# Kernel optimization log

Measured on AMD Instinct MI355X. Metric: run time of the kernel, lower is better.

The kernel has to match this reference:

```python
import jax, jax.numpy as jnp
import numpy as np

B, S, D, H = 2, 2048, 1024, 16
HD = D // H  # head_dim = 64


def setup_inputs() -> dict:
    key = jax.random.key(0)
    ks = jax.random.split(key, 5)
    scale = 0.02
    return {
        "x": jax.random.normal(ks[0], (B, S, D), dtype=jnp.float32),
        "q_w": jax.random.normal(ks[1], (D, D), dtype=jnp.float32) * scale,
        "k_w": jax.random.normal(ks[2], (D, D), dtype=jnp.float32) * scale,
        "v_w": jax.random.normal(ks[3], (D, D), dtype=jnp.float32) * scale,
        "o_w": jax.random.normal(ks[4], (D, D), dtype=jnp.float32) * scale,
    }


def _mhsa(x, q_w, k_w, v_w, o_w):
    b, s, d = x.shape
    # projections: weight is [out, in] as in torch Parameter usage
    Q = jnp.einsum('bsd,kd->bsk', x, q_w)
    K = jnp.einsum('bsd,kd->bsk', x, k_w)
    V = jnp.einsum('bsd,kd->bsk', x, v_w)
    # split heads: b s (h hd) -> b h s hd
    Q = Q.reshape(b, s, H, HD).transpose(0, 2, 1, 3)
    K = K.reshape(b, s, H, HD).transpose(0, 2, 1, 3)
    V = V.reshape(b, s, H, HD).transpose(0, 2, 1, 3)
    scores = jnp.einsum('bhqd,bhkd->bhqk', Q, K) / jnp.sqrt(jnp.float32(HD))
    causal = jnp.tril(jnp.ones((s, s), dtype=bool))  # [s, s]
    neg_inf = jnp.finfo(scores.dtype).min
    scores = jnp.where(causal[None, None], scores, neg_inf)
    attn = jax.nn.softmax(scores, axis=-1)
    O = jnp.einsum('bhqk,bhkd->bhqd', attn, V)
    O = O.transpose(0, 2, 1, 3).reshape(b, s, d)  # b h s hd -> b s (h hd)
    return jnp.einsum('bsv,dv->bsd', O, o_w)


def reference(x, q_w, k_w, v_w, o_w):
    return _mhsa(x, q_w, k_w, v_w, o_w)
```

## Files before the change

kernel.cpp:

```cpp
#include <hip/hip_runtime.h>


typedef __bf16 bf16x8 __attribute__((ext_vector_type(8)));
typedef float f32x4 __attribute__((ext_vector_type(4)));
typedef float f32x16 __attribute__((ext_vector_type(16)));

#define AS1 __attribute__((address_space(1)))
#define AS3 __attribute__((address_space(3)))

__device__ __forceinline__ ushort f2bf(float f) {
  unsigned u = __builtin_bit_cast(unsigned, f);
  u += 0x7fffu + ((u >> 16) & 1u);
  return (ushort)(u >> 16);
}

__device__ __forceinline__ unsigned cvt_pk_bf16(float lo, float hi) {
  unsigned r;
  asm("v_cvt_pk_bf16_f32 %0, %1, %2" : "=v"(r) : "v"(lo), "v"(hi));
  return r;
}

__device__ __forceinline__ float vexpf(float x) {
  float r;
  asm("v_exp_f32 %0, %1" : "=v"(r) : "v"(x));
  return r;
}

__device__ __forceinline__ bf16x8 ld16(const ushort* p) {
  return __builtin_bit_cast(bf16x8, *(const uint4*)p);
}

__device__ __forceinline__ void gload16(const ushort* g, ushort* l) {
  __builtin_amdgcn_global_load_lds((const AS1 void*)g, (AS3 void*)l, 16, 0, 0);
}

#define MFMA32(a, b, c) __builtin_amdgcn_mfma_f32_32x32x16_bf16(a, b, c, 0, 0, 0)

__global__ void cast_all(const float4* __restrict__ x, const float4* __restrict__ qw,
                         const float4* __restrict__ kw, const float4* __restrict__ vw,
                         const float4* __restrict__ ow, ushort4* __restrict__ out) {
  const int nx = 1 << 20;
  const int nw = 1 << 18;
  const float Cc = 0.125f * 1.44269504f;
  int stride = gridDim.x * blockDim.x;
  for (int i = blockIdx.x * blockDim.x + threadIdx.x; i < nx + 4 * nw; i += stride) {
    const float4* s;
    int off;
    float sc = 1.0f;
    if (i < nx) { s = x; off = i; }
    else {
      int j = i - nx, seg = j >> 18;
      off = j & (nw - 1);
      s = seg == 0 ? qw : seg == 1 ? kw : seg == 2 ? vw : ow;
      if (seg == 1) sc = Cc;
    }
    float4 v = s[off];
    ushort4 r;
    r.x = f2bf(v.x * sc); r.y = f2bf(v.y * sc); r.z = f2bf(v.z * sc); r.w = f2bf(v.w * sc);
    out[i] = r;
  }
}

template <bool F32OUT, int BN>
__device__ __forceinline__ void gemm_body(const ushort* __restrict__ A,
                                          const ushort* __restrict__ B,
                                          void* __restrict__ Cv,
                                          int bm, int bn, int N, int K,
                                          ushort* As, ushort* Bs) {
  const int tid = threadIdx.x;
  const int lane = tid & 63;
  const int wave = tid >> 6;
  const int r15 = lane & 15, hi = lane >> 4;
  const int wm = (wave >> 1) * 64, wn = (wave & 1) * (BN / 2);
  const int NJ = BN / 32;

  f32x4 acc[4][BN / 32] = {};

  const int KT = K >> 6;
  for (int kt = 0; kt < KT; ++kt) {
#pragma unroll
    for (int i = 0; i < 4; ++i) {
      int c = i * 256 + tid;
      int row = c >> 3, slot = c & 7;
      int coff = kt * 64 + ((((slot * 16) ^ ((row & 7) << 4))) >> 1);
      gload16(A + (size_t)(bm + row) * K + coff, As + c * 8);
    }
#pragma unroll
    for (int i = 0; i < BN / 32; ++i) {
      int c = i * 256 + tid;
      int row = c >> 3, slot = c & 7;
      int coff = kt * 64 + ((((slot * 16) ^ ((row & 7) << 4))) >> 1);
      gload16(B + (size_t)(bn + row) * K + coff, Bs + c * 8);
    }
    __syncthreads();
#pragma unroll
    for (int kc = 0; kc < 2; ++kc) {
      bf16x8 af[4], bfr[BN / 32];
#pragma unroll
      for (int mi = 0; mi < 4; ++mi) {
        int ra = wm + mi * 16 + r15;
        af[mi] = ld16(As + ra * 64 + ((kc * 32 + hi * 8) ^ ((ra & 7) << 3)));
      }
#pragma unroll
      for (int nj = 0; nj < NJ; ++nj) {
        int rb = wn + nj * 16 + r15;
        bfr[nj] = ld16(Bs + rb * 64 + ((kc * 32 + hi * 8) ^ ((rb & 7) << 3)));
      }
#pragma unroll
      for (int mi = 0; mi < 4; ++mi)
#pragma unroll
        for (int nj = 0; nj < NJ; ++nj)
          acc[mi][nj] = __builtin_amdgcn_mfma_f32_16x16x32_bf16(af[mi], bfr[nj], acc[mi][nj], 0, 0, 0);
    }
    __syncthreads();
  }

#pragma unroll
  for (int mi = 0; mi < 4; ++mi)
#pragma unroll
    for (int nj = 0; nj < NJ; ++nj) {
      int row = bm + wm + mi * 16 + hi * 4;
      int col = bn + wn + nj * 16 + r15;
#pragma unroll
      for (int j = 0; j < 4; ++j) {
        if (F32OUT)
          ((float*)Cv)[(size_t)(row + j) * N + col] = acc[mi][nj][j];
        else
          ((ushort*)Cv)[(size_t)(row + j) * N + col] = f2bf(acc[mi][nj][j]);
      }
    }
}

template <bool F32OUT, int BN>
__global__ __launch_bounds__(256) void gemm_nt(const ushort* __restrict__ A,
                                               const ushort* __restrict__ B,
                                               void* __restrict__ Cv,
                                               int M, int N, int K) {
  __shared__ ushort As[128 * 64];
  __shared__ ushort Bs[128 * 64];
  gemm_body<F32OUT, BN>(A, B, Cv, blockIdx.y * 128, blockIdx.x * BN, N, K, As, Bs);
}

__global__ __launch_bounds__(256) void gemm_qkvt(const ushort* __restrict__ xb,
                                                 const ushort* __restrict__ wqk,
                                                 const ushort* __restrict__ wv,
                                                 ushort* __restrict__ QKb,
                                                 ushort* __restrict__ VT) {
  __shared__ ushort As[128 * 64];
  __shared__ ushort Bs[128 * 64];
  if (blockIdx.x < 16)
    gemm_body<false, 128>(xb, wqk, QKb, blockIdx.y * 128, blockIdx.x * 128, 2048, 1024, As, Bs);
  else
    gemm_body<false, 128>(wv, xb, VT, (blockIdx.x - 16) * 128, blockIdx.y * 128, 4096, 1024, As, Bs);
}

__global__ __launch_bounds__(512, 4) void attn_fwd(const ushort* __restrict__ QK,
                                                   const ushort* __restrict__ VT,
                                                   ushort* __restrict__ Ob) {
  __shared__ __align__(16) ushort lds[33024];
  ushort* Ks0 = lds;
  ushort* Vs0 = lds + 16384;
  float* mlsh = (float*)(lds + 32768);
  float* osh = (float*)lds;

  const int tid = threadIdx.x, lane = tid & 63, wave = tid >> 6;
  const int l31 = lane & 31, hi = lane >> 5;
  const int kh = wave >> 2;
  const int hw = wave & 3;
  const int bh = blockIdx.x;
  const int y = blockIdx.y;
  const int qt = (y & 8) ? (15 - (y & 7)) : (y & 7);
  const int nh = 2 * (qt + 1);
  const size_t base = (size_t)(bh >> 4) * (2048 * 2048) + (bh & 15) * 64;
  const int qbase = qt * 128 + hw * 32;
  const int qrow = qbase + l31;
  const size_t KSTEP = (size_t)32 * 2048;

  bf16x8 qf[4];
  {
    const ushort* qp = QK + base + (size_t)qrow * 2048 + hi * 8;
#pragma unroll
    for (int c = 0; c < 4; ++c) qf[c] = ld16(qp + c * 16);
  }

  const int krow = tid >> 3, kslot = tid & 7;
  const int ksub = krow >> 5;
  const ushort* kg = QK + base + 1024 +
                     (size_t)((ksub * nh) * 32 + (krow & 31)) * 2048 +
                     ((((kslot * 16) ^ ((krow & 7) << 4))) >> 1);
  const int vd = tid >> 3;
  const int slotx = (tid & 7) ^ (vd & 7);
  const ushort* vgp = VT + (size_t)((bh & 15) * 64 + vd) * 4096 + (bh >> 4) * 2048 +
                      (size_t)((slotx >> 2) * nh) * 32 + (slotx & 3) * 8;

  f32x16 o0 = {}, o1 = {};
  float l_r = 0.f;

  {
    gload16(kg, Ks0 + tid * 8);
    gload16(vgp, Vs0 + tid * 8);
    gload16(kg + KSTEP, Ks0 + 4096 + tid * 8);
    gload16(vgp + 32, Vs0 + 4096 + tid * 8);
  }
  __syncthreads();

  for (int tt = 0; tt < nh; tt += 2) {
    const int pb = (tt >> 1) & 1;
    if (tt + 2 < nh) {
      gload16(kg + (size_t)(tt + 2) * KSTEP, Ks0 + (pb ^ 1) * 8192 + tid * 8);
      gload16(vgp + (size_t)(tt + 2) * 32, Vs0 + (pb ^ 1) * 8192 + tid * 8);
      gload16(kg + (size_t)(tt + 3) * KSTEP, Ks0 + (pb ^ 1) * 8192 + 4096 + tid * 8);
      gload16(vgp + (size_t)(tt + 3) * 32, Vs0 + (pb ^ 1) * 8192 + 4096 + tid * 8);
    }

#pragma unroll
    for (int u = 0; u < 2; ++u) {
      const int t = tt + u;
      const ushort* Kb = Ks0 + pb * 8192 + u * 4096;
      const ushort* Vb = Vs0 + pb * 8192 + u * 4096;
      const int kvb = (kh * nh + t) * 32;
      if (kvb <= qbase + 31) {
        f32x16 s = {};
        __builtin_amdgcn_s_setprio(1);
#pragma unroll
        for (int c = 0; c < 4; ++c) {
          int col = c * 16 + hi * 8;
          int r0 = kh * 32 + l31;
          bf16x8 k0 = ld16(Kb + r0 * 64 + (col ^ ((r0 & 7) << 3)));
          s = MFMA32(k0, qf[c], s);
        }
        __builtin_amdgcn_s_setprio(0);

        if (kvb + 31 > qbase) {
#pragma unroll
          for (int r = 0; r < 16; ++r) {
            int kvl = (r & 3) + 8 * (r >> 2) + 4 * hi;
            if (kvb + kvl > qrow) s[r] = -3e38f;
          }
        }

        float p[16];
#pragma unroll
        for (int r = 0; r < 16; ++r) p[r] = vexpf(s[r]);
        float ts[8];
#pragma unroll
        for (int r = 0; r < 8; ++r) ts[r] = p[r] + p[r + 8];
#pragma unroll
        for (int off = 4; off > 0; off >>= 1)
#pragma unroll
          for (int r = 0; r < off; ++r) ts[r] += ts[r + off];
        l_r += ts[0] + __shfl_xor(ts[0], 32);

#pragma unroll
        for (int c = 0; c < 2; ++c) {
          const int o = c * 8;
          unsigned a0 = cvt_pk_bf16(p[o + 0], p[o + 1]);
          unsigned a1 = cvt_pk_bf16(p[o + 2], p[o + 3]);
          unsigned b0 = cvt_pk_bf16(p[o + 4], p[o + 5]);
          unsigned b1 = cvt_pk_bf16(p[o + 6], p[o + 7]);
          asm("v_permlane32_swap_b32 %0, %1" : "+v"(a0), "+v"(b0));
          asm("v_permlane32_swap_b32 %0, %1" : "+v"(a1), "+v"(b1));
          uint4 y4;
          y4.x = a0;
          y4.y = a1;
          y4.z = b0;
          y4.w = b1;
          bf16x8 pf = __builtin_bit_cast(bf16x8, y4);

          int col = kh * 32 + c * 16 + hi * 8;
          int d0r = l31, d1r = 32 + l31;
          bf16x8 v0 = ld16(Vb + d0r * 64 + (col ^ ((d0r & 7) << 3)));
          bf16x8 v1 = ld16(Vb + d1r * 64 + (col ^ ((d1r & 7) << 3)));
          __builtin_amdgcn_s_setprio(1);
          o0 = MFMA32(v0, pf, o0);
          o1 = MFMA32(v1, pf, o1);
          __builtin_amdgcn_s_setprio(0);
        }
      }
    }

    __syncthreads();
  }

  if (kh) {
#pragma unroll
    for (int r = 0; r < 16; ++r) {
      osh[(hw * 32 + r) * 64 + lane] = o0[r];
      osh[(hw * 32 + 16 + r) * 64 + lane] = o1[r];
    }
    if (lane < 32) mlsh[hw * 32 + lane] = l_r;
  }
  __syncthreads();
  if (!kh) {
    float l_hi = mlsh[hw * 32 + l31];
    float lm = l_r + l_hi;
    float linv = lm > 0.f ? 1.0f / lm : 0.f;
#pragma unroll
    for (int r = 0; r < 16; ++r) {
      o0[r] = (o0[r] + osh[(hw * 32 + r) * 64 + lane]) * linv;
      o1[r] = (o1[r] + osh[(hw * 32 + 16 + r) * 64 + lane]) * linv;
    }
  }
  __syncthreads();
  if (!kh) {
    ushort* sm = lds;
    int q = hw * 32 + l31;
#pragma unroll
    for (int r = 0; r < 16; ++r) {
      int d = (r & 3) + 8 * (r >> 2) + 4 * hi;
      sm[q * 64 + (d ^ ((q & 7) << 3))] = f2bf(o0[r]);
      int d2 = d + 32;
      sm[q * 64 + (d2 ^ ((q & 7) << 3))] = f2bf(o1[r]);
    }
  }
  __syncthreads();
#pragma unroll
  for (int i = 0; i < 2; ++i) {
    int idx = i * 512 + tid;
    int row = idx >> 3, slot = idx & 7;
    uint4 v = *(const uint4*)(lds + row * 64 + ((slot * 8) ^ ((row & 7) << 3)));
    *(uint4*)(Ob + ((size_t)((bh >> 4) * 2048 + qt * 128 + row)) * 1024 +
              (bh & 15) * 64 + slot * 8) = v;
  }
}

extern "C" void kernel_launch(void* const* d_in, const int* in_sizes, int n_in,
                              void* d_out, int out_size, void* d_ws, size_t ws_size,
                              hipStream_t stream) {
  (void)in_sizes; (void)n_in; (void)out_size; (void)ws_size;
  const float* x = (const float*)d_in[0];
  const float* qw = (const float*)d_in[1];
  const float* kw = (const float*)d_in[2];
  const float* vw = (const float*)d_in[3];
  const float* ow = (const float*)d_in[4];
  float* out = (float*)d_out;

  const int NT = 4096;
  const int D = 1024;

  ushort* xb    = (ushort*)d_ws;
  ushort* wqkv  = xb + (size_t)NT * D;
  ushort* wob   = wqkv + (size_t)3 * D * D;
  ushort* QKb   = wob + (size_t)D * D;
  ushort* VT    = QKb + (size_t)NT * 2 * D;
  ushort* Ob    = VT + (size_t)D * NT;

  cast_all<<<2048, 256, 0, stream>>>((const float4*)x, (const float4*)qw,
                                     (const float4*)kw, (const float4*)vw,
                                     (const float4*)ow, (ushort4*)xb);

  gemm_qkvt<<<dim3(24, 32), 256, 0, stream>>>(xb, wqkv, wqkv + (size_t)2 * D * D, QKb, VT);

  attn_fwd<<<dim3(32, 16), 512, 0, stream>>>(QKb, VT, Ob);

  gemm_nt<true, 64><<<dim3(D / 64, NT / 128), 256, 0, stream>>>(Ob, wob, out, NT, D, D);
}
```

Baseline: 88.55 us.

## Give each attention wave two query sub-tiles and split KV four ways

Reorganizes attn_fwd so each wave handles 64 query rows (two 32-row sub-tiles) with the KV range split across four wave groups instead of two. Each K/V fragment read from LDS is reused for twice as many MFMAs, and the row-sum reduction is deferred to a per-register accumulator finished once after the loop. The cost is more accumulator registers (occupancy hint lowered from 4 to 2 blocks), larger LDS use, and a three-way cross-group merge of partial outputs at the end.

```diff
diff --git a/kernel.cpp b/kernel.cpp
--- a/kernel.cpp
+++ b/kernel.cpp
@@ -154,163 +154,194 @@
     gemm_body<false, 128>(wv, xb, VT, (blockIdx.x - 16) * 128, blockIdx.y * 128, 4096, 1024, As, Bs);
 }
 
-__global__ __launch_bounds__(512, 4) void attn_fwd(const ushort* __restrict__ QK,
+__global__ __launch_bounds__(512, 2) void attn_fwd(const ushort* __restrict__ QK,
                                                    const ushort* __restrict__ VT,
                                                    ushort* __restrict__ Ob) {
-  __shared__ __align__(16) ushort lds[33024];
+  __shared__ __align__(16) ushort lds[50176];
   ushort* Ks0 = lds;
   ushort* Vs0 = lds + 16384;
-  float* mlsh = (float*)(lds + 32768);
   float* osh = (float*)lds;
+  float* mlsh = (float*)(lds + 49152);
 
   const int tid = threadIdx.x, lane = tid & 63, wave = tid >> 6;
   const int l31 = lane & 31, hi = lane >> 5;
-  const int kh = wave >> 2;
-  const int hw = wave & 3;
+  const int kh = wave >> 1;
+  const int hw = wave & 1;
   const int bh = blockIdx.x;
   const int y = blockIdx.y;
   const int qt = (y & 8) ? (15 - (y & 7)) : (y & 7);
-  const int nh = 2 * (qt + 1);
+  const int nh = qt + 1;
   const size_t base = (size_t)(bh >> 4) * (2048 * 2048) + (bh & 15) * 64;
-  const int qbase = qt * 128 + hw * 32;
-  const int qrow = qbase + l31;
+  const int qbaseW = qt * 128 + hw * 64;
+  const int qrowA = qbaseW + l31;
+  const int qrowB = qbaseW + 32 + l31;
   const size_t KSTEP = (size_t)32 * 2048;
 
-  bf16x8 qf[4];
+  bf16x8 qfA[4], qfB[4];
   {
-    const ushort* qp = QK + base + (size_t)qrow * 2048 + hi * 8;
-#pragma unroll
-    for (int c = 0; c < 4; ++c) qf[c] = ld16(qp + c * 16);
+    const ushort* qpA = QK + base + (size_t)qrowA * 2048 + hi * 8;
+    const ushort* qpB = QK + base + (size_t)qrowB * 2048 + hi * 8;
+#pragma unroll
+    for (int c = 0; c < 4; ++c) { qfA[c] = ld16(qpA + c * 16); qfB[c] = ld16(qpB + c * 16); }
   }
 
   const int krow = tid >> 3, kslot = tid & 7;
   const int ksub = krow >> 5;
-  const ushort* kg = QK + base + 1024 +
-                     (size_t)((ksub * nh) * 32 + (krow & 31)) * 2048 +
-                     ((((kslot * 16) ^ ((krow & 7) << 4))) >> 1);
-  const int vd = tid >> 3;
-  const int slotx = (tid & 7) ^ (vd & 7);
-  const ushort* vgp = VT + (size_t)((bh & 15) * 64 + vd) * 4096 + (bh >> 4) * 2048 +
-                      (size_t)((slotx >> 2) * nh) * 32 + (slotx & 3) * 8;
-
-  f32x16 o0 = {}, o1 = {};
-  float l_r = 0.f;
-
+  const int kcol = ((((kslot * 16) ^ ((krow & 7) << 4))) >> 1);
+  const ushort* kg0 = QK + base + 1024 +
+                      (size_t)((ksub * nh) * 32 + (krow & 31)) * 2048 + kcol;
+  const ushort* kg1 = kg0 + (size_t)(2 * nh) * KSTEP;
+  const int vd0 = tid >> 4;
+  const int sgx = (tid & 15) ^ (vd0 & 7);
+  const int vstream = sgx >> 2, vkv = (sgx & 3) * 8;
+  const ushort* vg0 = VT + (size_t)((bh & 15) * 64 + vd0) * 4096 + (bh >> 4) * 2048 +
+                      (size_t)(vstream * nh) * 32 + vkv;
+  const ushort* vg1 = vg0 + (size_t)32 * 4096;
+
+  f32x16 o0A = {}, o1A = {}, o0B = {}, o1B = {};
+  f32x16 laccA = {}, laccB = {};
+
+  gload16(kg0, Ks0 + tid * 8);
+  gload16(kg1, Ks0 + (512 + tid) * 8);
+  gload16(vg0, Vs0 + tid * 8);
+  gload16(vg1, Vs0 + (512 + tid) * 8);
+  __syncthreads();
+
+  for (int t = 0; t < nh; ++t) {
+    const int buf = t & 1;
+    if (t + 1 < nh) {
+      gload16(kg0 + (size_t)(t + 1) * KSTEP, Ks0 + (buf ^ 1) * 8192 + tid * 8);
+      gload16(kg1 + (size_t)(t + 1) * KSTEP, Ks0 + (buf ^ 1) * 8192 + (512 + tid) * 8);
+      gload16(vg0 + (size_t)(t + 1) * 32, Vs0 + (buf ^ 1) * 8192 + tid * 8);
+      gload16(vg1 + (size_t)(t + 1) * 32, Vs0 + (buf ^ 1) * 8192 + (512 + tid) * 8);
+    }
+
+    const ushort* Kb = Ks0 + buf * 8192;
+    const ushort* Vb = Vs0 + buf * 8192;
+    const int kvb = (kh * nh + t) * 32;
+    if (kvb <= qbaseW + 63) {
+      f32x16 sA = {}, sB = {};
+      __builtin_amdgcn_s_setprio(1);
+#pragma unroll
+      for (int c = 0; c < 4; ++c) {
+        int col = c * 16 + hi * 8;
+        int r0 = kh * 32 + l31;
+        bf16x8 k0 = ld16(Kb + r0 * 64 + (col ^ ((r0 & 7) << 3)));
+        sA = MFMA32(k0, qfA[c], sA);
+        sB = MFMA32(k0, qfB[c], sB);
+      }
+      __builtin_amdgcn_s_setprio(0);
+
+      if (kvb + 31 > qbaseW) {
+#pragma unroll
+        for (int r = 0; r < 16; ++r) {
+          int kvl = (r & 3) + 8 * (r >> 2) + 4 * hi;
+          if (kvb + kvl > qrowA) sA[r] = -3e38f;
+          if (kvb + kvl > qrowB) sB[r] = -3e38f;
+        }
+      }
+
+      float pA[16], pB[16];
+#pragma unroll
+      for (int r = 0; r < 16; ++r) { pA[r] = vexpf(sA[r]); laccA[r] += pA[r]; }
+#pragma unroll
+      for (int r = 0; r < 16; ++r) { pB[r] = vexpf(sB[r]); laccB[r] += pB[r]; }
+
+#pragma unroll
+      for (int c = 0; c < 2; ++c) {
+        const int o = c * 8;
+        unsigned aA0 = cvt_pk_bf16(pA[o + 0], pA[o + 1]);
+        unsigned aA1 = cvt_pk_bf16(pA[o + 2], pA[o + 3]);
+        unsigned bA0 = cvt_pk_bf16(pA[o + 4], pA[o + 5]);
+        unsigned bA1 = cvt_pk_bf16(pA[o + 6], pA[o + 7]);
+        asm("v_permlane32_swap_b32 %0, %1" : "+v"(aA0), "+v"(bA0));
+        asm("v_permlane32_swap_b32 %0, %1" : "+v"(aA1), "+v"(bA1));
+        uint4 yA; yA.x = aA0; yA.y = aA1; yA.z = bA0; yA.w = bA1;
+        bf16x8 pfA = __builtin_bit_cast(bf16x8, yA);
+
+        unsigned aB0 = cvt_pk_bf16(pB[o + 0], pB[o + 1]);
+        unsigned aB1 = cvt_pk_bf16(pB[o + 2], pB[o + 3]);
+        unsigned bB0 = cvt_pk_bf16(pB[o + 4], pB[o + 5]);
+        unsigned bB1 = cvt_pk_bf16(pB[o + 6], pB[o + 7]);
+        asm("v_permlane32_swap_b32 %0, %1" : "+v"(aB0), "+v"(bB0));
+        asm("v_permlane32_swap_b32 %0, %1" : "+v"(aB1), "+v"(bB1));
+        uint4 yB; yB.x = aB0; yB.y = aB1; yB.z = bB0; yB.w = bB1;
+        bf16x8 pfB = __builtin_bit_cast(bf16x8, yB);
+
+        int col = kh * 32 + c * 16 + hi * 8;
+        int d0r = l31, d1r = 32 + l31;
+        bf16x8 v0 = ld16(Vb + d0r * 128 + (col ^ ((d0r & 7) << 3)));
+        bf16x8 v1 = ld16(Vb + d1r * 128 + (col ^ ((d1r & 7) << 3)));
+        __builtin_amdgcn_s_setprio(1);
+        o0A = MFMA32(v0, pfA, o0A);
+        o1A = MFMA32(v1, pfA, o1A);
+        o0B = MFMA32(v0, pfB, o0B);
+        o1B = MFMA32(v1, pfB, o1B);
+        __builtin_amdgcn_s_setprio(0);
+      }
+    }
+
+    __syncthreads();
+  }
+
+  float lA_r, lB_r;
   {
-    gload16(kg, Ks0 + tid * 8);
-    gload16(vgp, Vs0 + tid * 8);
-    gload16(kg + KSTEP, Ks0 + 4096 + tid * 8);
-    gload16(vgp + 32, Vs0 + 4096 + tid * 8);
-  }
-  __syncthreads();
-
-  for (int tt = 0; tt < nh; tt += 2) {
-    const int pb = (tt >> 1) & 1;
-    if (tt + 2 < nh) {
-      gload16(kg + (size_t)(tt + 2) * KSTEP, Ks0 + (pb ^ 1) * 8192 + tid * 8);
-      gload16(vgp + (size_t)(tt + 2) * 32, Vs0 + (pb ^ 1) * 8192 + tid * 8);
-      gload16(kg + (size_t)(tt + 3) * KSTEP, Ks0 + (pb ^ 1) * 8192 + 4096 + tid * 8);
-      gload16(vgp + (size_t)(tt + 3) * 32, Vs0 + (pb ^ 1) * 8192 + 4096 + tid * 8);
-    }
-
-#pragma unroll
-    for (int u = 0; u < 2; ++u) {
-      const int t = tt + u;
-      const ushort* Kb = Ks0 + pb * 8192 + u * 4096;
-      const ushort* Vb = Vs0 + pb * 8192 + u * 4096;
-      const int kvb = (kh * nh + t) * 32;
-      if (kvb <= qbase + 31) {
-        f32x16 s = {};
-        __builtin_amdgcn_s_setprio(1);
-#pragma unroll
-        for (int c = 0; c < 4; ++c) {
-          int col = c * 16 + hi * 8;
-          int r0 = kh * 32 + l31;
-          bf16x8 k0 = ld16(Kb + r0 * 64 + (col ^ ((r0 & 7) << 3)));
-          s = MFMA32(k0, qf[c], s);
-        }
-        __builtin_amdgcn_s_setprio(0);
-
-        if (kvb + 31 > qbase) {
-#pragma unroll
-          for (int r = 0; r < 16; ++r) {
-            int kvl = (r & 3) + 8 * (r >> 2) + 4 * hi;
-            if (kvb + kvl > qrow) s[r] = -3e38f;
-          }
-        }
-
-        float p[16];
-#pragma unroll
-        for (int r = 0; r < 16; ++r) p[r] = vexpf(s[r]);
-        float ts[8];
-#pragma unroll
-        for (int r = 0; r < 8; ++r) ts[r] = p[r] + p[r + 8];
-#pragma unroll
-        for (int off = 4; off > 0; off >>= 1)
-#pragma unroll
-          for (int r = 0; r < off; ++r) ts[r] += ts[r + off];
-        l_r += ts[0] + __shfl_xor(ts[0], 32);
-
-#pragma unroll
-        for (int c = 0; c < 2; ++c) {
-          const int o = c * 8;
-          unsigned a0 = cvt_pk_bf16(p[o + 0], p[o + 1]);
-          unsigned a1 = cvt_pk_bf16(p[o + 2], p[o + 3]);
-          unsigned b0 = cvt_pk_bf16(p[o + 4], p[o + 5]);
-          unsigned b1 = cvt_pk_bf16(p[o + 6], p[o + 7]);
-          asm("v_permlane32_swap_b32 %0, %1" : "+v"(a0), "+v"(b0));
-          asm("v_permlane32_swap_b32 %0, %1" : "+v"(a1), "+v"(b1));
-          uint4 y4;
-          y4.x = a0;
-          y4.y = a1;
-          y4.z = b0;
-          y4.w = b1;
-          bf16x8 pf = __builtin_bit_cast(bf16x8, y4);
-
-          int col = kh * 32 + c * 16 + hi * 8;
-          int d0r = l31, d1r = 32 + l31;
-          bf16x8 v0 = ld16(Vb + d0r * 64 + (col ^ ((d0r & 7) << 3)));
-          bf16x8 v1 = ld16(Vb + d1r * 64 + (col ^ ((d1r & 7) << 3)));
-          __builtin_amdgcn_s_setprio(1);
-          o0 = MFMA32(v0, pf, o0);
-          o1 = MFMA32(v1, pf, o1);
-          __builtin_amdgcn_s_setprio(0);
-        }
-      }
-    }
-
-    __syncthreads();
-  }
-
+    float ta[8], tb[8];
+#pragma unroll
+    for (int r = 0; r < 8; ++r) { ta[r] = laccA[r] + laccA[r + 8]; tb[r] = laccB[r] + laccB[r + 8]; }
+#pragma unroll
+    for (int off = 4; off > 0; off >>= 1)
+#pragma unroll
+      for (int r = 0; r < off; ++r) { ta[r] += ta[r + off]; tb[r] += tb[r + off]; }
+    lA_r = ta[0] + __shfl_xor(ta[0], 32);
+    lB_r = tb[0] + __shfl_xor(tb[0], 32);
+  }
+
+  __syncthreads();
   if (kh) {
+    const int mb = (kh - 1) * 128 + hw * 64;
 #pragma unroll
     for (int r = 0; r < 16; ++r) {
-      osh[(hw * 32 + r) * 64 + lane] = o0[r];
-      osh[(hw * 32 + 16 + r) * 64 + lane] = o1[r];
-    }
-    if (lane < 32) mlsh[hw * 32 + lane] = l_r;
+      osh[(mb + r) * 64 + lane] = o0A[r];
+      osh[(mb + 16 + r) * 64 + lane] = o1A[r];
+      osh[(mb + 32 + r) * 64 + lane] = o0B[r];
+      osh[(mb + 48 + r) * 64 + lane] = o1B[r];
+    }
+    if (lane < 32) {
+      mlsh[(kh - 1) * 128 + hw * 64 + l31] = lA_r;
+      mlsh[(kh - 1) * 128 + hw * 64 + 32 + l31] = lB_r;
+    }
   }
   __syncthreads();
   if (!kh) {
-    float l_hi = mlsh[hw * 32 + l31];
-    float lm = l_r + l_hi;
-    float linv = lm > 0.f ? 1.0f / lm : 0.f;
+    const int mb = hw * 64;
+    float lmA = lA_r + mlsh[mb + l31] + mlsh[128 + mb + l31] + mlsh[256 + mb + l31];
+    float lmB = lB_r + mlsh[mb + 32 + l31] + mlsh[128 + mb + 32 + l31] + mlsh[256 + mb + 32 + l31];
+    float liA = lmA > 0.f ? 1.0f / lmA : 0.f;
+    float liB = lmB > 0.f ? 1.0f / lmB : 0.f;
 #pragma unroll
     for (int r = 0; r < 16; ++r) {
-      o0[r] = (o0[r] + osh[(hw * 32 + r) * 64 + lane]) * linv;
-      o1[r] = (o1[r] + osh[(hw * 32 + 16 + r) * 64 + lane]) * linv;
+      o0A[r] = (o0A[r] + osh[(mb + r) * 64 + lane] + osh[(128 + mb + r) * 64 + lane] +
+                osh[(256 + mb + r) * 64 + lane]) * liA;
+      o1A[r] = (o1A[r] + osh[(mb + 16 + r) * 64 + lane] + osh[(128 + mb + 16 + r) * 64 + lane] +
+                osh[(256 + mb + 16 + r) * 64 + lane]) * liA;
+      o0B[r] = (o0B[r] + osh[(mb + 32 + r) * 64 + lane] + osh[(128 + mb + 32 + r) * 64 + lane] +
+                osh[(256 + mb + 32 + r) * 64 + lane]) * liB;
+      o1B[r] = (o1B[r] + osh[(mb + 48 + r) * 64 + lane] + osh[(128 + mb + 48 + r) * 64 + lane] +
+                osh[(256 + mb + 48 + r) * 64 + lane]) * liB;
     }
   }
   __syncthreads();
   if (!kh) {
     ushort* sm = lds;
-    int q = hw * 32 + l31;
+    int qA = hw * 64 + l31, qB = qA + 32;
 #pragma unroll
     for (int r = 0; r < 16; ++r) {
       int d = (r & 3) + 8 * (r >> 2) + 4 * hi;
-      sm[q * 64 + (d ^ ((q & 7) << 3))] = f2bf(o0[r]);
-      int d2 = d + 32;
-      sm[q * 64 + (d2 ^ ((q & 7) << 3))] = f2bf(o1[r]);
+      sm[qA * 64 + (d ^ ((qA & 7) << 3))] = f2bf(o0A[r]);
+      sm[qA * 64 + ((d + 32) ^ ((qA & 7) << 3))] = f2bf(o1A[r]);
+      sm[qB * 64 + (d ^ ((qB & 7) << 3))] = f2bf(o0B[r]);
+      sm[qB * 64 + ((d + 32) ^ ((qB & 7) << 3))] = f2bf(o1B[r]);
     }
   }
   __syncthreads();
```

Measured after the change: 92.20 us. 1.04x slower.
